# Kernel tuning notes

Measured on AMD Instinct MI355X. Metric: run time of the kernel, lower is better.

The kernel has to match this reference:

```python
import jax, jax.numpy as jnp
import numpy as np

B, T, IN, H, L = 262144, 30, 1, 5, 5  # batch, seq_len, input_size, hidden_size, num_layers


def setup_inputs() -> dict:
    key = jax.random.key(0)
    ks = jax.random.split(key, 9)
    s = 1.0 / np.sqrt(H)  # PyTorch GRU init: U(-1/sqrt(H), 1/sqrt(H))
    u = lambda k, shape: jax.random.uniform(k, shape, jnp.float32, -s, s)
    return {
        "x": jax.random.normal(ks[0], (B, IN, T), jnp.float32),
        "w_ih0": u(ks[1], (2, 3 * H, IN)),      # layer 0, [dir, 3H, in]
        "w_hh0": u(ks[2], (2, 3 * H, H)),
        "b_ih0": u(ks[3], (2, 3 * H)),
        "b_hh0": u(ks[4], (2, 3 * H)),
        "w_ih": u(ks[5], (L - 1, 2, 3 * H, 2 * H)),  # layers 1..4 consume bidir output (2H)
        "w_hh": u(ks[6], (L - 1, 2, 3 * H, H)),
        "b_ih": u(ks[7], (L - 1, 2, 3 * H)),
        "b_hh": u(ks[8], (L - 1, 2, 3 * H)),
    }


def _gru_dir(x_seq, w_ih, w_hh, b_ih, b_hh, reverse):
    """Single-direction GRU over x_seq [B, T, D] -> outputs [B, T, H] (PyTorch gate math)."""
    def step(h, x_t):
        gi = x_t @ w_ih.T + b_ih            # [B, 3H]
        gh = h @ w_hh.T + b_hh              # [B, 3H]
        i_r, i_z, i_n = jnp.split(gi, 3, axis=-1)
        h_r, h_z, h_n = jnp.split(gh, 3, axis=-1)
        r = jax.nn.sigmoid(i_r + h_r)
        z = jax.nn.sigmoid(i_z + h_z)
        n = jnp.tanh(i_n + r * h_n)
        h_new = (1.0 - z) * n + z * h
        return h_new, h_new

    h0 = jnp.zeros((x_seq.shape[0], w_hh.shape[1]), x_seq.dtype)
    # scan over time; reverse=True matches PyTorch's reverse direction (output kept in
    # original time order, ys[t] = hidden after consuming x[T-1..t]).
    _, ys = jax.lax.scan(step, h0, jnp.swapaxes(x_seq, 0, 1), reverse=reverse)
    return jnp.swapaxes(ys, 0, 1)


def reference(x, w_ih0, w_hh0, b_ih0, b_hh0, w_ih, w_hh, b_ih, b_hh):
    h = jnp.transpose(x, (0, 2, 1))  # [B, C, T] -> [B, T, C]
    wih = [w_ih0] + [w_ih[l] for l in range(w_ih.shape[0])]
    whh = [w_hh0] + [w_hh[l] for l in range(w_hh.shape[0])]
    bih = [b_ih0] + [b_ih[l] for l in range(b_ih.shape[0])]
    bhh = [b_hh0] + [b_hh[l] for l in range(b_hh.shape[0])]
    for l in range(len(wih)):
        fwd = _gru_dir(h, wih[l][0], whh[l][0], bih[l][0], bhh[l][0], False)
        bwd = _gru_dir(h, wih[l][1], whh[l][1], bih[l][1], bhh[l][1], True)
        h = jnp.concatenate([fwd, bwd], axis=-1)  # [B, T, 2H]
    return h[:, -1:, :]  # out[:, -1, :].unsqueeze(1) -> [B, 1, 2H]
```

## Files before the change

kernel.cpp:

```cpp
#include <hip/hip_runtime.h>


#define NB 262144
#define T 30
#define NBLK (NB / 32)
#define SEQW (T * 5 * 32)

typedef _Float16 f16x8 __attribute__((ext_vector_type(8)));
typedef float f32x16 __attribute__((ext_vector_type(16)));

__device__ unsigned g_seq[(unsigned long long)NBLK * SEQW];

#define SIG_SCALE  (-1.4426950408889634f)
#define TANH_SCALE ( 2.8853900817779268f)

__device__ __forceinline__ float sig_s(float xs) {
    return __builtin_amdgcn_rcpf(1.0f + __builtin_amdgcn_exp2f(xs));
}
__device__ __forceinline__ float tanh_s(float xs) {
    return fmaf(-2.0f, __builtin_amdgcn_rcpf(1.0f + __builtin_amdgcn_exp2f(xs)), 1.0f);
}
__device__ __forceinline__ unsigned hbits(_Float16 a) {
    union { _Float16 f; unsigned short s; } u; u.f = a;
    return (unsigned)u.s;
}
__device__ __forceinline__ unsigned packh(_Float16 a, _Float16 b) {
    return hbits(a) | (hbits(b) << 16);
}

template <bool IS_L0, int NT, bool WRITE, bool STORE, bool G_R>
__device__ __forceinline__ void run_layer(
    const float* __restrict__ wih, const float* __restrict__ whh,
    const float* __restrict__ bih, const float* __restrict__ bhh,
    const unsigned* seqR, unsigned* seqW, const float* xg,
    float* outp, const int d, const int lane)
{
    const int lr   = lane & 31;
    const int half = lane >> 5;

    const int u_r = lr >> 2;
    const int g   = lr & 3;
    const bool rv = lr < 20;

    f16x8 af;
#pragma unroll
    for (int e = 0; e < 8; e++) {
        const int k = 8 * half + e;
        float v = 0.f;
        if (rv) {
            if (!IS_L0) {
                if (k <= 4 || (k >= 8 && k <= 12)) {
                    const int idx = (k < 8) ? k : (k - 3);
                    const int j = (idx & 1) * 5 + (idx >> 1);
                    if (g == 0)      v = SIG_SCALE  * wih[u_r * 10 + j];
                    else if (g == 1) v = SIG_SCALE  * wih[(5 + u_r) * 10 + j];
                    else if (g == 2) v = TANH_SCALE * wih[(10 + u_r) * 10 + j];
                } else if (k >= 5 && k <= 7) {
                    const int uh = 2 * (k - 5);
                    if (g == 0)      v = SIG_SCALE  * whh[u_r * 5 + uh];
                    else if (g == 1) v = SIG_SCALE  * whh[(5 + u_r) * 5 + uh];
                    else if (g == 3) v = TANH_SCALE * whh[(10 + u_r) * 5 + uh];
                } else if (k == 13 || k == 14) {
                    const int uh = 2 * (k - 13) + 1;
                    if (g == 0)      v = SIG_SCALE  * whh[u_r * 5 + uh];
                    else if (g == 1) v = SIG_SCALE  * whh[(5 + u_r) * 5 + uh];
                    else if (g == 3) v = TANH_SCALE * whh[(10 + u_r) * 5 + uh];
                }
            } else {
                if (k == 0) {
                    if (g == 0)      v = SIG_SCALE  * wih[u_r];
                    else if (g == 1) v = SIG_SCALE  * wih[5 + u_r];
                    else if (g == 2) v = TANH_SCALE * wih[10 + u_r];
                } else if (k >= 5 && k <= 7) {
                    const int uh = 2 * (k - 5);
                    if (g == 0)      v = SIG_SCALE  * whh[u_r * 5 + uh];
                    else if (g == 1) v = SIG_SCALE  * whh[(5 + u_r) * 5 + uh];
                    else if (g == 3) v = TANH_SCALE * whh[(10 + u_r) * 5 + uh];
                } else if (k == 13 || k == 14) {
                    const int uh = 2 * (k - 13) + 1;
                    if (g == 0)      v = SIG_SCALE  * whh[u_r * 5 + uh];
                    else if (g == 1) v = SIG_SCALE  * whh[(5 + u_r) * 5 + uh];
                    else if (g == 3) v = TANH_SCALE * whh[(10 + u_r) * 5 + uh];
                }
            }
        }
        af[e] = (_Float16)v;
    }

    f32x16 bc;
#pragma unroll
    for (int q = 0; q < 4; q++) {
        const int u = 2 * q + half;
        float b0 = 0.f, b1 = 0.f, b2 = 0.f, b3 = 0.f;
        if (q < 3 && u < 5) {
            b0 = SIG_SCALE  * (bih[u] + bhh[u]);
            b1 = SIG_SCALE  * (bih[5 + u] + bhh[5 + u]);
            b2 = TANH_SCALE * bih[10 + u];
            b3 = TANH_SCALE * bhh[10 + u];
        }
        bc[4 * q + 0] = b0; bc[4 * q + 1] = b1;
        bc[4 * q + 2] = b2; bc[4 * q + 3] = b3;
    }

    const unsigned S01 = half ? 0x05040302u : 0x03020100u;
    const unsigned S2  = half ? 0x05040302u : 0x05040100u;

    const int sdir = d ? -1 : 1;
    const int p0   = d ? (T - 1) : 0;
    const unsigned* rbase = seqR + p0 * 160 + lr + (half ? 64 : 0);
    _Float16* wbase = (_Float16*)seqW + p0 * 320 + lr * 2 + d;
    const int rstep = sdir * 160, wstep = sdir * 320;

    float h0 = 0.f, h1 = 0.f, h2 = 0.f;
    unsigned hw2 = 0, hw3 = 0;

    auto step = [&](unsigned pa, unsigned pb, unsigned pc, unsigned xv) {
        union { f16x8 v; unsigned u[4]; } B;
        if constexpr (!IS_L0) {
            B.u[0] = __builtin_amdgcn_perm(pb, pa, S01);
            B.u[1] = __builtin_amdgcn_perm(pc, pb, S01);
            B.u[2] = __builtin_amdgcn_perm(hw2, pc, S2);
        } else {
            B.u[0] = half ? 0u : xv;
            B.u[1] = 0u;
            B.u[2] = hw2 << 16;
        }
        B.u[3] = hw3;

        const f32x16 D = __builtin_amdgcn_mfma_f32_32x32x16_f16(af, B.v, bc, 0, 0, 0);

        float r, z, n;
        r = sig_s(D[0]); z = sig_s(D[1]);
        n = tanh_s(fmaf(r, D[3], D[2]));
        h0 = fmaf(z, h0 - n, n);
        r = sig_s(D[4]); z = sig_s(D[5]);
        n = tanh_s(fmaf(r, D[7], D[6]));
        h1 = fmaf(z, h1 - n, n);
        r = sig_s(D[8]); z = sig_s(D[9]);
        n = tanh_s(fmaf(r, D[11], D[10]));
        h2 = fmaf(z, h2 - n, n);

        const _Float16 q0f = (_Float16)h0, q1f = (_Float16)h1, q2f = (_Float16)h2;
        hw2 = hbits(q0f);
        hw3 = packh(q1f, q2f);

        if constexpr (WRITE) {
            wbase[half * 64]       = q0f;
            wbase[(2 + half) * 64] = q1f;
            if (!half) wbase[4 * 64] = q2f;
            wbase += wstep;
        }
    };

    if constexpr (IS_L0) {
        const float* xp = xg + lr * T + p0;
        float xf = *xp;
        for (int s = 0; s < NT; s++) {
            const unsigned xv = hbits((_Float16)xf);
            if (s + 1 < NT) { xp += sdir; xf = *xp; }
            step(0u, 0u, 0u, xv);
        }
    } else if constexpr (!G_R) {
        const unsigned* rb = rbase;
        unsigned a0 = rb[0], a1 = rb[32], a2 = rb[64];
        for (int s = 0; s < NT; s++) {
            const unsigned t0 = a0, t1 = a1, t2 = a2;
            if (s + 1 < NT) {
                rb += rstep;
                a0 = rb[0]; a1 = rb[32]; a2 = rb[64];
            }
            step(t0, t1, t2, 0u);
        }
    } else if constexpr (NT == 1) {
        step(rbase[0], rbase[32], rbase[64], 0u);
    } else {
        const unsigned* rn = rbase;
        unsigned a0 = rn[0], a1 = rn[32], a2 = rn[64];
        rn += rstep;
        unsigned b0 = rn[0], b1 = rn[32], b2 = rn[64];
        rn += rstep;
        for (int s = 0; s < NT; s += 2) {
            step(a0, a1, a2, 0u);
            if (s + 2 < NT) {
                a0 = rn[0]; a1 = rn[32]; a2 = rn[64];
                rn += rstep;
            }
            step(b0, b1, b2, 0u);
            if (s + 3 < NT) {
                b0 = rn[0]; b1 = rn[32]; b2 = rn[64];
                rn += rstep;
            }
        }
    }

    if constexpr (STORE) {
        outp[half]     = h0;
        outp[2 + half] = h1;
        if (!half) outp[4] = h2;
    }
}

__global__ void __launch_bounds__(128, 4) gru_all(
    const float* __restrict__ x,
    const float* __restrict__ wih0, const float* __restrict__ whh0,
    const float* __restrict__ bih0, const float* __restrict__ bhh0,
    const float* __restrict__ wihL, const float* __restrict__ whhL,
    const float* __restrict__ bihL, const float* __restrict__ bhhL,
    float* __restrict__ out)
{
    __shared__ unsigned S[T][5][32];

    const int tid  = threadIdx.x;
    const int d    = tid >> 6;
    const int lane = tid & 63;
    const int lr   = lane & 31;
    const long base = (long)blockIdx.x * 32;

    const float* xg = x + base * T;
    unsigned* G = g_seq + (unsigned long long)blockIdx.x * SEQW;

    run_layer<true, T, true, false, false>(
        wih0 + d * 15, whh0 + d * 75, bih0 + d * 15, bhh0 + d * 15,
        nullptr, &S[0][0][0], xg, nullptr, d, lane);
    __syncthreads();

    run_layer<false, T, true, false, false>(
        wihL + (0 + d) * 150, whhL + (0 + d) * 75, bihL + (0 + d) * 15, bhhL + (0 + d) * 15,
        &S[0][0][0], G, nullptr, nullptr, d, lane);
    __syncthreads();

    run_layer<false, T, true, false, true>(
        wihL + (2 + d) * 150, whhL + (2 + d) * 75, bihL + (2 + d) * 15, bhhL + (2 + d) * 15,
        G, &S[0][0][0], nullptr, nullptr, d, lane);
    __syncthreads();

    run_layer<false, T, true, false, false>(
        wihL + (4 + d) * 150, whhL + (4 + d) * 75, bihL + (4 + d) * 15, bhhL + (4 + d) * 15,
        &S[0][0][0], G, nullptr, nullptr, d, lane);
    __syncthreads();

    {
        float* op = out + (base + lr) * 10 + d * 5;
        if (d == 0)
            run_layer<false, T, false, true, true>(
                wihL + 6 * 150, whhL + 6 * 75, bihL + 6 * 15, bhhL + 6 * 15,
                G, nullptr, nullptr, op, d, lane);
        else
            run_layer<false, 1, false, true, true>(
                wihL + 7 * 150, whhL + 7 * 75, bihL + 7 * 15, bhhL + 7 * 15,
                G, nullptr, nullptr, op, d, lane);
    }
}

extern "C" void kernel_launch(void* const* d_in, const int* in_sizes, int n_in,
                              void* d_out, int out_size, void* d_ws, size_t ws_size,
                              hipStream_t stream) {
    const float* x    = (const float*)d_in[0];
    const float* wih0 = (const float*)d_in[1];
    const float* whh0 = (const float*)d_in[2];
    const float* bih0 = (const float*)d_in[3];
    const float* bhh0 = (const float*)d_in[4];
    const float* wihL = (const float*)d_in[5];
    const float* whhL = (const float*)d_in[6];
    const float* bihL = (const float*)d_in[7];
    const float* bhhL = (const float*)d_in[8];
    float* out = (float*)d_out;

    gru_all<<<NBLK, 128, 0, stream>>>(x, wih0, whh0, bih0, bhh0,
                                      wihL, whhL, bihL, bhhL, out);
}
```

Measured before the change: 437.3 us.

## Process two 32-row batch tiles per wave to interleave independent GRU recurrences

Measured after the change: 497.4 us. 13.7% more time.

```diff
diff --git a/kernel.cpp b/kernel.cpp
--- a/kernel.cpp
+++ b/kernel.cpp
@@ -3,8 +3,8 @@
 
 #define NB 262144
 #define T 30
-#define NBLK (NB / 32)
-#define SEQW (T * 5 * 32)
+#define NBLK (NB / 64)
+#define SEQW (T * 5 * 64)
 
 typedef _Float16 f16x8 __attribute__((ext_vector_type(8)));
 typedef float f32x16 __attribute__((ext_vector_type(16)));
@@ -107,100 +107,134 @@
 
     const int sdir = d ? -1 : 1;
     const int p0   = d ? (T - 1) : 0;
-    const unsigned* rbase = seqR + p0 * 160 + lr + (half ? 64 : 0);
-    _Float16* wbase = (_Float16*)seqW + p0 * 320 + lr * 2 + d;
-    const int rstep = sdir * 160, wstep = sdir * 320;
-
-    float h0 = 0.f, h1 = 0.f, h2 = 0.f;
-    unsigned hw2 = 0, hw3 = 0;
-
-    auto step = [&](unsigned pa, unsigned pb, unsigned pc, unsigned xv) {
-        union { f16x8 v; unsigned u[4]; } B;
+    const unsigned* rbA = seqR + p0 * 320 + lr + (half ? 128 : 0);
+    _Float16* wbase = (_Float16*)seqW + p0 * 640 + lr * 2 + d;
+    const int rstep = sdir * 320, wstep = sdir * 640;
+
+    float h0A = 0.f, h1A = 0.f, h2A = 0.f;
+    float h0B = 0.f, h1B = 0.f, h2B = 0.f;
+    unsigned hw2A = 0, hw3A = 0, hw2B = 0, hw3B = 0;
+
+    auto stepAB = [&](unsigned paA, unsigned pbA, unsigned pcA,
+                      unsigned paB, unsigned pbB, unsigned pcB,
+                      unsigned xvA, unsigned xvB) {
+        union { f16x8 v; unsigned u[4]; } BA, BB;
         if constexpr (!IS_L0) {
-            B.u[0] = __builtin_amdgcn_perm(pb, pa, S01);
-            B.u[1] = __builtin_amdgcn_perm(pc, pb, S01);
-            B.u[2] = __builtin_amdgcn_perm(hw2, pc, S2);
+            BA.u[0] = __builtin_amdgcn_perm(pbA, paA, S01);
+            BA.u[1] = __builtin_amdgcn_perm(pcA, pbA, S01);
+            BA.u[2] = __builtin_amdgcn_perm(hw2A, pcA, S2);
+            BB.u[0] = __builtin_amdgcn_perm(pbB, paB, S01);
+            BB.u[1] = __builtin_amdgcn_perm(pcB, pbB, S01);
+            BB.u[2] = __builtin_amdgcn_perm(hw2B, pcB, S2);
         } else {
-            B.u[0] = half ? 0u : xv;
-            B.u[1] = 0u;
-            B.u[2] = hw2 << 16;
-        }
-        B.u[3] = hw3;
-
-        const f32x16 D = __builtin_amdgcn_mfma_f32_32x32x16_f16(af, B.v, bc, 0, 0, 0);
+            BA.u[0] = half ? 0u : xvA; BA.u[1] = 0u; BA.u[2] = hw2A << 16;
+            BB.u[0] = half ? 0u : xvB; BB.u[1] = 0u; BB.u[2] = hw2B << 16;
+        }
+        BA.u[3] = hw3A;
+        BB.u[3] = hw3B;
+
+        const f32x16 DA = __builtin_amdgcn_mfma_f32_32x32x16_f16(af, BA.v, bc, 0, 0, 0);
+        const f32x16 DB = __builtin_amdgcn_mfma_f32_32x32x16_f16(af, BB.v, bc, 0, 0, 0);
 
         float r, z, n;
-        r = sig_s(D[0]); z = sig_s(D[1]);
-        n = tanh_s(fmaf(r, D[3], D[2]));
-        h0 = fmaf(z, h0 - n, n);
-        r = sig_s(D[4]); z = sig_s(D[5]);
-        n = tanh_s(fmaf(r, D[7], D[6]));
-        h1 = fmaf(z, h1 - n, n);
-        r = sig_s(D[8]); z = sig_s(D[9]);
-        n = tanh_s(fmaf(r, D[11], D[10]));
-        h2 = fmaf(z, h2 - n, n);
-
-        const _Float16 q0f = (_Float16)h0, q1f = (_Float16)h1, q2f = (_Float16)h2;
-        hw2 = hbits(q0f);
-        hw3 = packh(q1f, q2f);
+        r = sig_s(DA[0]); z = sig_s(DA[1]);
+        n = tanh_s(fmaf(r, DA[3], DA[2]));
+        h0A = fmaf(z, h0A - n, n);
+        r = sig_s(DA[4]); z = sig_s(DA[5]);
+        n = tanh_s(fmaf(r, DA[7], DA[6]));
+        h1A = fmaf(z, h1A - n, n);
+        r = sig_s(DA[8]); z = sig_s(DA[9]);
+        n = tanh_s(fmaf(r, DA[11], DA[10]));
+        h2A = fmaf(z, h2A - n, n);
+
+        r = sig_s(DB[0]); z = sig_s(DB[1]);
+        n = tanh_s(fmaf(r, DB[3], DB[2]));
+        h0B = fmaf(z, h0B - n, n);
+        r = sig_s(DB[4]); z = sig_s(DB[5]);
+        n = tanh_s(fmaf(r, DB[7], DB[6]));
+        h1B = fmaf(z, h1B - n, n);
+        r = sig_s(DB[8]); z = sig_s(DB[9]);
+        n = tanh_s(fmaf(r, DB[11], DB[10]));
+        h2B = fmaf(z, h2B - n, n);
+
+        const _Float16 q0A = (_Float16)h0A, q1A = (_Float16)h1A, q2A = (_Float16)h2A;
+        const _Float16 q0B = (_Float16)h0B, q1B = (_Float16)h1B, q2B = (_Float16)h2B;
+        hw2A = hbits(q0A); hw3A = packh(q1A, q2A);
+        hw2B = hbits(q0B); hw3B = packh(q1B, q2B);
 
         if constexpr (WRITE) {
-            wbase[half * 64]       = q0f;
-            wbase[(2 + half) * 64] = q1f;
-            if (!half) wbase[4 * 64] = q2f;
+            wbase[half * 128]       = q0A;
+            wbase[(2 + half) * 128] = q1A;
+            if (!half) wbase[4 * 128] = q2A;
+            _Float16* wb2 = wbase + 64;
+            wb2[half * 128]       = q0B;
+            wb2[(2 + half) * 128] = q1B;
+            if (!half) wb2[4 * 128] = q2B;
             wbase += wstep;
         }
     };
 
     if constexpr (IS_L0) {
-        const float* xp = xg + lr * T + p0;
-        float xf = *xp;
+        const float* xpA = xg + lr * T + p0;
+        const float* xpB = xpA + 32 * T;
+        float xfA = *xpA, xfB = *xpB;
         for (int s = 0; s < NT; s++) {
-            const unsigned xv = hbits((_Float16)xf);
-            if (s + 1 < NT) { xp += sdir; xf = *xp; }
-            step(0u, 0u, 0u, xv);
+            const unsigned xvA = hbits((_Float16)xfA);
+            const unsigned xvB = hbits((_Float16)xfB);
+            if (s + 1 < NT) { xpA += sdir; xfA = *xpA; xpB += sdir; xfB = *xpB; }
+            stepAB(0u, 0u, 0u, 0u, 0u, 0u, xvA, xvB);
         }
     } else if constexpr (!G_R) {
-        const unsigned* rb = rbase;
-        unsigned a0 = rb[0], a1 = rb[32], a2 = rb[64];
+        const unsigned* rb = rbA;
+        unsigned a0 = rb[0], a1 = rb[64], a2 = rb[128];
+        unsigned a3 = rb[32], a4 = rb[96], a5 = rb[160];
         for (int s = 0; s < NT; s++) {
-            const unsigned t0 = a0, t1 = a1, t2 = a2;
+            const unsigned t0 = a0, t1 = a1, t2 = a2, t3 = a3, t4 = a4, t5 = a5;
             if (s + 1 < NT) {
                 rb += rstep;
-                a0 = rb[0]; a1 = rb[32]; a2 = rb[64];
+                a0 = rb[0]; a1 = rb[64]; a2 = rb[128];
+                a3 = rb[32]; a4 = rb[96]; a5 = rb[160];
             }
-            step(t0, t1, t2, 0u);
+            stepAB(t0, t1, t2, t3, t4, t5, 0u, 0u);
         }
     } else if constexpr (NT == 1) {
-        step(rbase[0], rbase[32], rbase[64], 0u);
+        stepAB(rbA[0], rbA[64], rbA[128], rbA[32], rbA[96], rbA[160], 0u, 0u);
     } else {
-        const unsigned* rn = rbase;
-        unsigned a0 = rn[0], a1 = rn[32], a2 = rn[64];
+        const unsigned* rn = rbA;
+        unsigned a0 = rn[0], a1 = rn[64], a2 = rn[128];
+        unsigned a3 = rn[32], a4 = rn[96], a5 = rn[160];
         rn += rstep;
-        unsigned b0 = rn[0], b1 = rn[32], b2 = rn[64];
+        unsigned b0 = rn[0], b1 = rn[64], b2 = rn[128];
+        unsigned b3 = rn[32], b4 = rn[96], b5 = rn[160];
         rn += rstep;
         for (int s = 0; s < NT; s += 2) {
-            step(a0, a1, a2, 0u);
+            stepAB(a0, a1, a2, a3, a4, a5, 0u, 0u);
             if (s + 2 < NT) {
-                a0 = rn[0]; a1 = rn[32]; a2 = rn[64];
+                a0 = rn[0]; a1 = rn[64]; a2 = rn[128];
+                a3 = rn[32]; a4 = rn[96]; a5 = rn[160];
                 rn += rstep;
             }
-            step(b0, b1, b2, 0u);
+            stepAB(b0, b1, b2, b3, b4, b5, 0u, 0u);
             if (s + 3 < NT) {
-                b0 = rn[0]; b1 = rn[32]; b2 = rn[64];
+                b0 = rn[0]; b1 = rn[64]; b2 = rn[128];
+                b3 = rn[32]; b4 = rn[96]; b5 = rn[160];
                 rn += rstep;
             }
         }
     }
 
     if constexpr (STORE) {
-        outp[half]     = h0;
-        outp[2 + half] = h1;
-        if (!half) outp[4] = h2;
-    }
-}
-
-__global__ void __launch_bounds__(128, 4) gru_all(
+        outp[half]     = h0A;
+        outp[2 + half] = h1A;
+        if (!half) outp[4] = h2A;
+        float* op2 = outp + 320;
+        op2[half]     = h0B;
+        op2[2 + half] = h1B;
+        if (!half) op2[4] = h2B;
+    }
+}
+
+__global__ void __launch_bounds__(128, 2) gru_all(
     const float* __restrict__ x,
     const float* __restrict__ wih0, const float* __restrict__ whh0,
     const float* __restrict__ bih0, const float* __restrict__ bhh0,
@@ -208,13 +242,13 @@
     const float* __restrict__ bihL, const float* __restrict__ bhhL,
     float* __restrict__ out)
 {
-    __shared__ unsigned S[T][5][32];
+    __shared__ unsigned S[T][5][64];
 
     const int tid  = threadIdx.x;
     const int d    = tid >> 6;
     const int lane = tid & 63;
     const int lr   = lane & 31;
-    const long base = (long)blockIdx.x * 32;
+    const long base = (long)blockIdx.x * 64;
 
     const float* xg = x + base * T;
     unsigned* G = g_seq + (unsigned long long)blockIdx.x * SEQW;
```
